# Kernel tuning notes

Measured on AMD Instinct MI355X. Metric: run time of the kernel, lower is better.

The kernel has to match this reference:

```python
import jax, jax.numpy as jnp
import numpy as np

B, S, D, H = 2, 2048, 2048, 16
HD = D // H          # 128
HALF = HD // 2       # 64
EPS = 1e-6


def setup_inputs() -> dict:
    key = jax.random.key(0)
    ks = jax.random.split(key, 10)
    x = jax.random.normal(ks[0], (B, S, D), jnp.float32)
    # RoPE frequencies: standard theta=10000, per (position, half head dim)
    inv_freq = 1.0 / (10000.0 ** (np.arange(HALF, dtype=np.float64) / HALF))
    ang = np.outer(np.arange(S, dtype=np.float64), inv_freq)  # (S, HALF)
    freqs_cos = jnp.asarray(np.cos(ang), jnp.float32)[:, None, :]  # (S,1,HALF)
    freqs_sin = jnp.asarray(np.sin(ang), jnp.float32)[:, None, :]
    sc = 0.02
    qw = jax.random.normal(ks[1], (D, D), jnp.float32) * sc
    kw = jax.random.normal(ks[2], (D, D), jnp.float32) * sc
    vw = jax.random.normal(ks[3], (D, D), jnp.float32) * sc
    ow = jax.random.normal(ks[4], (D, D), jnp.float32) * sc
    qb = jax.random.normal(ks[5], (D,), jnp.float32) * sc
    kb = jax.random.normal(ks[6], (D,), jnp.float32) * sc
    vb = jax.random.normal(ks[7], (D,), jnp.float32) * sc
    ob = jax.random.normal(ks[8], (D,), jnp.float32) * sc
    qnorm_w = jnp.ones((D,), jnp.float32)
    knorm_w = jnp.ones((D,), jnp.float32)
    return {"x": x, "freqs_cos": freqs_cos, "freqs_sin": freqs_sin,
            "qw": qw, "qb": qb, "kw": kw, "kb": kb, "vw": vw, "vb": vb,
            "ow": ow, "ob": ob, "qnorm_w": qnorm_w, "knorm_w": knorm_w}


def _rmsnorm(h, w):
    # norm in fp32 over full last dim (dim, not per-head), as in the source
    hf = h.astype(jnp.float32)
    inv = jax.lax.rsqrt(jnp.mean(hf * hf, axis=-1, keepdims=True) + EPS)
    return (hf * inv).astype(h.dtype) * w


def _rope(h, cos, sin):
    # h: (B,S,D) -> complex rotation on interleaved pairs per head
    b, s, _ = h.shape
    hp = h.reshape(b, s, H, HALF, 2)
    x1, x2 = hp[..., 0], hp[..., 1]
    c = cos[None]   # (1,S,1,HALF) broadcasts over batch & heads
    sn = sin[None]
    o1 = x1 * c - x2 * sn
    o2 = x1 * sn + x2 * c
    return jnp.stack([o1, o2], axis=-1).reshape(b, s, H * HD)


def reference(x, freqs_cos, freqs_sin, qw, qb, kw, kb, vw, vb, ow, ob, qnorm_w, knorm_w):
    q = _rope(_rmsnorm(x @ qw.T + qb, qnorm_w), freqs_cos, freqs_sin)
    k = _rope(_rmsnorm(x @ kw.T + kb, knorm_w), freqs_cos, freqs_sin)
    v = x @ vw.T + vb
    b, s, _ = x.shape
    qh = q.reshape(b, s, H, HD)
    kh = k.reshape(b, s, H, HD)
    vh = v.reshape(b, s, H, HD)
    scale = 1.0 / jnp.sqrt(jnp.float32(HD))
    att = jnp.einsum('bqhd,bkhd->bhqk', qh, kh) * scale
    p = jax.nn.softmax(att, axis=-1)
    o = jnp.einsum('bhqk,bkhd->bqhd', p, vh).reshape(b, s, D)
    return o @ ow.T + ob
```

## Files before the change

kernel.cpp:

```cpp
#include <hip/hip_runtime.h>
#include <stdint.h>

#define B_SZ 2
#define S_LEN 2048
#define D_DIM 2048
#define NHEAD 16
#define HD 128
#define HALF 64
#define MROWS (B_SZ * S_LEN)

typedef __attribute__((ext_vector_type(8))) __bf16 bf16x8;
typedef __attribute__((ext_vector_type(8))) unsigned short u16x8;
typedef __attribute__((ext_vector_type(4))) float f32x4;
typedef __attribute__((ext_vector_type(16))) float f32x16;
typedef __attribute__((ext_vector_type(4))) unsigned int u32x4;

__device__ inline unsigned short f2bf(float x) {
  union { float f; uint32_t u; } c; c.f = x;
  uint32_t r = (c.u + 0x7fffu + ((c.u >> 16) & 1u)) >> 16;
  return (unsigned short)r;
}

__device__ inline float bf2f(unsigned short b) {
  union { uint32_t u; float f; } c; c.u = (uint32_t)b << 16;
  return c.f;
}

__device__ inline void gll16(const void* g, void* l) {
  __builtin_amdgcn_global_load_lds(
      (const __attribute__((address_space(1))) void*)g,
      (__attribute__((address_space(3))) void*)l,
      16, 0, 0);
}

__global__ void cast_all(const float* __restrict__ x,
                         const float* __restrict__ qw, const float* __restrict__ kw,
                         const float* __restrict__ vw, const float* __restrict__ ow,
                         unsigned short* __restrict__ xb,
                         unsigned short* __restrict__ qwb, unsigned short* __restrict__ kwb,
                         unsigned short* __restrict__ vwb, unsigned short* __restrict__ owb) {
  const int n_x = (MROWS * D_DIM) / 4;
  const int n_w = (D_DIM * D_DIM) / 4;
  const int total = n_x + 4 * n_w;
  int i = blockIdx.x * blockDim.x + threadIdx.x;
  int stride = gridDim.x * blockDim.x;
  for (; i < total; i += stride) {
    const float* src; unsigned short* dst; int off;
    if (i < n_x) { src = x; dst = xb; off = i; }
    else {
      int j = i - n_x;
      int seg = j >> 20;
      off = j & (n_w - 1);
      src = seg == 0 ? qw : seg == 1 ? kw : seg == 2 ? vw : ow;
      dst = seg == 0 ? qwb : seg == 1 ? kwb : seg == 2 ? vwb : owb;
    }
    float4 v = reinterpret_cast<const float4*>(src)[off];
    ushort4 o;
    o.x = f2bf(v.x); o.y = f2bf(v.y); o.z = f2bf(v.z); o.w = f2bf(v.w);
    reinterpret_cast<ushort4*>(dst)[off] = o;
  }
}

template <int MODE>
__global__ __launch_bounds__(256) void gemm_bt(
    const unsigned short* __restrict__ A, const unsigned short* __restrict__ Bt,
    const float* __restrict__ bias, void* __restrict__ Cv,
    int M, int N, int K) {
  __shared__ __align__(16) unsigned short As[128 * 32];
  __shared__ __align__(16) unsigned short Bs[128 * 32];
  const int tid = threadIdx.x;
  const int lane = tid & 63;
  const int wave = tid >> 6;
  const int nbn = N >> 7;
  const int chunk = gridDim.x >> 3;
  const int lin = (blockIdx.x & 7) * chunk + (blockIdx.x >> 3);
  const int bm = lin / nbn, bn = lin - bm * nbn;
  const int wr = wave >> 1, wc = wave & 1;
  const int lm = lane & 15, lg = lane >> 4;

  f32x4 acc[4][4] = {};

  for (int k0 = 0; k0 < K; k0 += 32) {
    __syncthreads();
#pragma unroll
    for (int j = 0; j < 2; ++j) {
      int ob = wave * 2048 + j * 1024;
      int o = ob + lane * 16;
      int row = o >> 6;
      int col = (o & 63) >> 1;
      const unsigned short* ga = A + (size_t)(bm * 128 + row) * K + k0 + col;
      gll16(ga, (char*)As + ob);
      const unsigned short* gb = Bt + (size_t)(bn * 128 + row) * K + k0 + col;
      gll16(gb, (char*)Bs + ob);
    }
    __syncthreads();

    bf16x8 af[4], bfr[4];
#pragma unroll
    for (int mi = 0; mi < 4; ++mi)
      af[mi] = *reinterpret_cast<const bf16x8*>(
          &As[(wr * 64 + mi * 16 + lm) * 32 + lg * 8]);
#pragma unroll
    for (int ni = 0; ni < 4; ++ni)
      bfr[ni] = *reinterpret_cast<const bf16x8*>(
          &Bs[(wc * 64 + ni * 16 + lm) * 32 + lg * 8]);
#pragma unroll
    for (int mi = 0; mi < 4; ++mi)
#pragma unroll
      for (int ni = 0; ni < 4; ++ni)
        acc[mi][ni] = __builtin_amdgcn_mfma_f32_16x16x32_bf16(
            af[mi], bfr[ni], acc[mi][ni], 0, 0, 0);
  }

#pragma unroll
  for (int ni = 0; ni < 4; ++ni) {
    int col = bn * 128 + wc * 64 + ni * 16 + lm;
    float bv = bias[col];
    if constexpr (MODE == 2) {
      int h = col >> 7, d = col & (HD - 1);
#pragma unroll
      for (int mi = 0; mi < 4; ++mi) {
        int row0 = bm * 128 + wr * 64 + mi * 16 + lg * 4;
        int b = row0 >> 11, s0 = row0 & (S_LEN - 1);
        ushort4 o;
        o.x = f2bf(acc[mi][ni][0] + bv);
        o.y = f2bf(acc[mi][ni][1] + bv);
        o.z = f2bf(acc[mi][ni][2] + bv);
        o.w = f2bf(acc[mi][ni][3] + bv);
        unsigned short* vt = (unsigned short*)Cv;
        size_t oi = ((((size_t)(b * NHEAD + h) * (S_LEN / 64) + (s0 >> 6)) * HD + d) << 6)
                    + (s0 & 63);
        *reinterpret_cast<ushort4*>(vt + oi) = o;
      }
    } else {
#pragma unroll
      for (int mi = 0; mi < 4; ++mi) {
#pragma unroll
        for (int r = 0; r < 4; ++r) {
          int row = bm * 128 + wr * 64 + mi * 16 + lg * 4 + r;
          float v = acc[mi][ni][r] + bv;
          if constexpr (MODE == 1)
            ((unsigned short*)Cv)[(size_t)row * N + col] = f2bf(v);
          else
            ((float*)Cv)[(size_t)row * N + col] = v;
        }
      }
    }
  }
}

template <int BLOCKED>
__global__ __launch_bounds__(256) void norm_rope(
    const unsigned short* __restrict__ h, const float* __restrict__ w,
    const float* __restrict__ cosb, const float* __restrict__ sinb,
    unsigned short* __restrict__ out, float outscale) {
  const int row = blockIdx.x;
  const int pos = row & (S_LEN - 1);
  const unsigned short* hr = h + (size_t)row * D_DIM;
  const int t = threadIdx.x;
  const int d = t * 8;

  u16x8 hv = *reinterpret_cast<const u16x8*>(hr + d);
  float a[8];
#pragma unroll
  for (int i = 0; i < 8; ++i) a[i] = bf2f(hv[i]);
  float ss = 0.f;
#pragma unroll
  for (int i = 0; i < 8; ++i) ss += a[i] * a[i];
#pragma unroll
  for (int off = 32; off > 0; off >>= 1) ss += __shfl_down(ss, off);
  __shared__ float red[4];
  if ((t & 63) == 0) red[t >> 6] = ss;
  __syncthreads();
  float tot = red[0] + red[1] + red[2] + red[3];
  float inv = rsqrtf(tot * (1.0f / D_DIM) + 1e-6f) * outscale;

  const int p = (d & (HD - 1)) >> 1;
  const float* cp = cosb + pos * HALF + p;
  const float* sp = sinb + pos * HALF + p;
  const float* wp = w + d;

  float c0 = cp[0], c1 = cp[1], c2 = cp[2], c3 = cp[3];
  float s0 = sp[0], s1 = sp[1], s2 = sp[2], s3 = sp[3];
#pragma unroll
  for (int i = 0; i < 8; ++i) a[i] = a[i] * inv * wp[i];
  u16x8 o;
  o[0] = f2bf(a[0] * c0 - a[1] * s0);
  o[1] = f2bf(a[0] * s0 + a[1] * c0);
  o[2] = f2bf(a[2] * c1 - a[3] * s1);
  o[3] = f2bf(a[2] * s1 + a[3] * c1);
  o[4] = f2bf(a[4] * c2 - a[5] * s2);
  o[5] = f2bf(a[4] * s2 + a[5] * c2);
  o[6] = f2bf(a[6] * c3 - a[7] * s3);
  o[7] = f2bf(a[6] * s3 + a[7] * c3);
  if constexpr (BLOCKED) {
    int hh = t >> 4;
    int dd = d & (HD - 1);
    size_t oi = (((size_t)((row >> 11) * NHEAD + hh) * S_LEN) + pos) * HD + dd;
    *reinterpret_cast<u16x8*>(out + oi) = o;
  } else {
    *reinterpret_cast<u16x8*>(out + (size_t)row * D_DIM + d) = o;
  }
}

__global__ __launch_bounds__(512) void attn_kernel(
    const unsigned short* __restrict__ Q, const unsigned short* __restrict__ Kh,
    const unsigned short* __restrict__ Vt, unsigned short* __restrict__ O) {
  const int idx = blockIdx.x;
  const int swz = (idx & 7) * 32 + (idx >> 3);
  const int qb = swz & 7;
  const int h = (swz >> 3) & 15;
  const int b = swz >> 7;

  const int tid = threadIdx.x;
  const int lane = tid & 63;
  const int wave = tid >> 6;
  const int l31 = lane & 31;
  const int hh = lane >> 5;

  const size_t qbase = (size_t)b * S_LEN * D_DIM + (size_t)h * HD;
  const size_t hbase = (size_t)(b * NHEAD + h) * S_LEN * HD;
  const int q0w = qb * 256 + wave * 32;

  __shared__ __align__(16) unsigned short Ks[2 * 64 * 128];
  __shared__ __align__(16) unsigned short Vs[128 * 64];

  bf16x8 qf[8];
#pragma unroll
  for (int ds_ = 0; ds_ < 8; ++ds_)
    qf[ds_] = *reinterpret_cast<const bf16x8*>(
        Q + qbase + (size_t)(q0w + l31) * D_DIM + ds_ * 16 + hh * 8);

  f32x16 oacc[4] = {};
  float mrow = -1e30f, lrow = 0.f;

  const int pbase = wave * 1024 + (lane << 4);

  auto stageK = [&](int buf, int tix) {
    const unsigned short* ksrc = Kh + hbase + (size_t)tix * (64 * HD);
#pragma unroll
    for (int j = 0; j < 2; ++j) {
      int p = pbase + j * 8192;
      int kr = p >> 8;
      int kc = ((p >> 4) & 15) ^ ((kr & 7) ^ ((kr >> 3) & 7));
      gll16(ksrc + kr * 128 + kc * 8, (char*)Ks + buf * 16384 + p);
    }
  };
  auto stageV = [&](int tix) {
    const unsigned short* vsrc = Vt + hbase + (size_t)tix * (64 * HD);
#pragma unroll
    for (int j = 0; j < 2; ++j) {
      int p = pbase + j * 8192;
      int vr = p >> 7;
      int vc = ((p >> 4) & 7) ^ (((vr & 7) ^ ((vr >> 3) & 7)) & 7);
      gll16(vsrc + vr * 64 + vc * 8, (char*)Vs + p);
    }
  };

  stageK(0, 0);

  const int NT = S_LEN / 64;
  for (int t = 0; t < NT; ++t) {
    const int cur = t & 1;
    stageV(t);
    stageK(cur ^ 1, (t + 1 < NT) ? t + 1 : t);
    asm volatile("s_waitcnt vmcnt(4)" ::: "memory");
    __builtin_amdgcn_sched_barrier(0);
    __builtin_amdgcn_s_barrier();
    __builtin_amdgcn_sched_barrier(0);

    const char* kbp = (const char*)Ks + cur * 16384;
    const int fk0 = (l31 & 7) ^ ((l31 >> 3) & 7);
    const int fk1 = (l31 & 7) ^ (((l31 + 32) >> 3) & 7);
    f32x16 pA = {}, pB = {};
    __builtin_amdgcn_s_setprio(1);
#pragma unroll
    for (int ds_ = 0; ds_ < 8; ++ds_) {
      bf16x8 k0 = *reinterpret_cast<const bf16x8*>(
          kbp + l31 * 256 + (((ds_ * 2 + hh) ^ fk0) << 4));
      bf16x8 k1 = *reinterpret_cast<const bf16x8*>(
          kbp + (32 + l31) * 256 + (((ds_ * 2 + hh) ^ fk1) << 4));
      pA = __builtin_amdgcn_mfma_f32_32x32x16_bf16(k0, qf[ds_], pA, 0, 0, 0);
      pB = __builtin_amdgcn_mfma_f32_32x32x16_bf16(k1, qf[ds_], pB, 0, 0, 0);
    }
    __builtin_amdgcn_s_setprio(0);

    float m8[8];
#pragma unroll
    for (int r = 0; r < 8; ++r)
      m8[r] = fmaxf(fmaxf(pA[r], pA[r + 8]), fmaxf(pB[r], pB[r + 8]));
#pragma unroll
    for (int r = 0; r < 4; ++r) m8[r] = fmaxf(m8[r], m8[r + 4]);
    float mx = fmaxf(fmaxf(m8[0], m8[1]), fmaxf(m8[2], m8[3]));
    mx = fmaxf(mx, __shfl_xor(mx, 32));
    if (__any(mx > mrow + 8.0f)) {
      float nm = fmaxf(mrow, mx);
      float alpha = exp2f(mrow - nm);
      mrow = nm;
      lrow *= alpha;
#pragma unroll
      for (int r = 0; r < 16; ++r) {
        int qr = (r & 3) + 8 * (r >> 2) + 4 * hh;
        float av = __shfl(alpha, qr);
        oacc[0][r] *= av; oacc[1][r] *= av; oacc[2][r] *= av; oacc[3][r] *= av;
      }
    }
#pragma unroll
    for (int r = 0; r < 16; ++r) pA[r] = exp2f(pA[r] - mrow);
#pragma unroll
    for (int r = 0; r < 16; ++r) pB[r] = exp2f(pB[r] - mrow);
    float s8[8];
#pragma unroll
    for (int r = 0; r < 8; ++r)
      s8[r] = (pA[r] + pA[r + 8]) + (pB[r] + pB[r + 8]);
#pragma unroll
    for (int r = 0; r < 4; ++r) s8[r] += s8[r + 4];
    lrow += (s8[0] + s8[1]) + (s8[2] + s8[3]);

    uint32_t w[16];
#pragma unroll
    for (int gg = 0; gg < 4; ++gg) {
      uint32_t lo, hi;
      float a0 = pA[4 * gg], a1 = pA[4 * gg + 1], a2 = pA[4 * gg + 2], a3 = pA[4 * gg + 3];
      asm("v_cvt_pk_bf16_f32 %0, %1, %2" : "=v"(lo) : "v"(a0), "v"(a1));
      asm("v_cvt_pk_bf16_f32 %0, %1, %2" : "=v"(hi) : "v"(a2), "v"(a3));
      w[gg * 2] = lo; w[gg * 2 + 1] = hi;
    }
#pragma unroll
    for (int gg = 0; gg < 4; ++gg) {
      uint32_t lo, hi;
      float a0 = pB[4 * gg], a1 = pB[4 * gg + 1], a2 = pB[4 * gg + 2], a3 = pB[4 * gg + 3];
      asm("v_cvt_pk_bf16_f32 %0, %1, %2" : "=v"(lo) : "v"(a0), "v"(a1));
      asm("v_cvt_pk_bf16_f32 %0, %1, %2" : "=v"(hi) : "v"(a2), "v"(a3));
      w[8 + gg * 2] = lo; w[8 + gg * 2 + 1] = hi;
    }
    bf16x8 pa[4];
#pragma unroll
    for (int s = 0; s < 4; ++s) {
      int wb = (s >> 1) * 8 + (s & 1) * 4;
      uint32_t le = w[wb], he = w[wb + 1], lo_ = w[wb + 2], ho = w[wb + 3];
      asm("v_permlane32_swap_b32 %0, %1" : "+v"(le), "+v"(lo_));
      asm("v_permlane32_swap_b32 %0, %1" : "+v"(he), "+v"(ho));
      u32x4 fr = {le, he, lo_, ho};
      pa[s] = __builtin_bit_cast(bf16x8, fr);
    }

    asm volatile("s_waitcnt vmcnt(2)" ::: "memory");
    __builtin_amdgcn_sched_barrier(0);
    __builtin_amdgcn_s_barrier();
    __builtin_amdgcn_sched_barrier(0);

    const char* vbp = (const char*)Vs;
    __builtin_amdgcn_s_setprio(1);
#pragma unroll
    for (int db = 0; db < 4; ++db) {
      int d = db * 32 + l31;
      int fv = (d & 7) ^ ((d >> 3) & 7);
#pragma unroll
      for (int ks = 0; ks < 4; ++ks) {
        bf16x8 vv = *reinterpret_cast<const bf16x8*>(
            vbp + d * 128 + (((ks * 2 + hh) ^ fv) << 4));
        oacc[db] = __builtin_amdgcn_mfma_f32_32x32x16_bf16(pa[ks], vv, oacc[db], 0, 0, 0);
      }
    }
    __builtin_amdgcn_s_setprio(0);

    __builtin_amdgcn_sched_barrier(0);
    __builtin_amdgcn_s_barrier();
    __builtin_amdgcn_sched_barrier(0);
  }

  lrow += __shfl_xor(lrow, 32);
  float inv_[16];
#pragma unroll
  for (int r = 0; r < 16; ++r) {
    int qr = (r & 3) + 8 * (r >> 2) + 4 * hh;
    inv_[r] = 1.0f / __shfl(lrow, qr);
  }
#pragma unroll
  for (int db = 0; db < 4; ++db) {
#pragma unroll
    for (int r = 0; r < 16; ++r) {
      int qr = (r & 3) + 8 * (r >> 2) + 4 * hh;
      O[qbase + (size_t)(q0w + qr) * D_DIM + db * 32 + l31] =
          f2bf(oacc[db][r] * inv_[r]);
    }
  }
}

extern "C" void kernel_launch(void* const* d_in, const int* in_sizes, int n_in,
                              void* d_out, int out_size, void* d_ws, size_t ws_size,
                              hipStream_t stream) {
  const float* x   = (const float*)d_in[0];
  const float* fc  = (const float*)d_in[1];
  const float* fs  = (const float*)d_in[2];
  const float* qw  = (const float*)d_in[3];
  const float* qb  = (const float*)d_in[4];
  const float* kw  = (const float*)d_in[5];
  const float* kb  = (const float*)d_in[6];
  const float* vw  = (const float*)d_in[7];
  const float* vb  = (const float*)d_in[8];
  const float* ow  = (const float*)d_in[9];
  const float* ob  = (const float*)d_in[10];
  const float* qnw = (const float*)d_in[11];
  const float* knw = (const float*)d_in[12];
  float* out = (float*)d_out;

  const size_t MSD = (size_t)MROWS * D_DIM;
  const size_t WSZ = (size_t)D_DIM * D_DIM;
  char* ws = (char*)d_ws;
  unsigned short* xb   = (unsigned short*)ws; ws += MSD * 2;
  unsigned short* qwb  = (unsigned short*)ws; ws += WSZ * 2;
  unsigned short* kwb  = (unsigned short*)ws; ws += WSZ * 2;
  unsigned short* vwb  = (unsigned short*)ws; ws += WSZ * 2;
  unsigned short* owb  = (unsigned short*)ws; ws += WSZ * 2;
  unsigned short* qpre = (unsigned short*)ws; ws += MSD * 2;
  unsigned short* qb16 = (unsigned short*)ws; ws += MSD * 2;
  unsigned short* kb16 = (unsigned short*)ws; ws += MSD * 2;
  unsigned short* vt16 = (unsigned short*)ws; ws += MSD * 2;
  unsigned short* ob16 = (unsigned short*)ws; ws += MSD * 2;

  cast_all<<<2048, 256, 0, stream>>>(x, qw, kw, vw, ow, xb, qwb, kwb, vwb, owb);

  dim3 ggrid((D_DIM / 128) * (MROWS / 128));
  gemm_bt<2><<<ggrid, 256, 0, stream>>>(xb, vwb, vb, vt16, MROWS, D_DIM, D_DIM);
  gemm_bt<1><<<ggrid, 256, 0, stream>>>(xb, qwb, qb, qpre, MROWS, D_DIM, D_DIM);
  const float qscale = 0.08838834764831845f * 1.4426950408889634f;
  norm_rope<0><<<MROWS, 256, 0, stream>>>(qpre, qnw, fc, fs, qb16, qscale);
  gemm_bt<1><<<ggrid, 256, 0, stream>>>(xb, kwb, kb, qpre, MROWS, D_DIM, D_DIM);
  norm_rope<1><<<MROWS, 256, 0, stream>>>(qpre, knw, fc, fs, kb16, 1.0f);

  attn_kernel<<<dim3(S_LEN / 256 * NHEAD * B_SZ), 512, 0, stream>>>(qb16, kb16, vt16, ob16);

  gemm_bt<0><<<ggrid, 256, 0, stream>>>(ob16, owb, ob, out, MROWS, D_DIM, D_DIM);
}
```

Measured before the change: 339.6 us.

## Fuse QKV projections into one GEMM, merge norm-rope, widen attention KV tile

Runs the Q, K and V projections as a single GEMM with N=3*D by treating the contiguous qwb/kwb/vwb buffers as one weight matrix and copying the three biases into one contiguous buffer. Each output segment is routed to its own destination, with V still written in its blocked transposed layout. The two norm_rope launches become one kernel that chooses Q or K by block index. Separately, the attention kernel now processes 128 keys per iteration instead of 64, which doubles the K/V shared memory and the register use for scores in exchange for fewer barriers and loop iterations.

Result: faster. 324.3 us (-4.5%).

```diff
diff --git a/kernel.cpp b/kernel.cpp
--- a/kernel.cpp
+++ b/kernel.cpp
@@ -64,7 +64,8 @@
 template <int MODE>
 __global__ __launch_bounds__(256) void gemm_bt(
     const unsigned short* __restrict__ A, const unsigned short* __restrict__ Bt,
-    const float* __restrict__ bias, void* __restrict__ Cv,
+    const float* __restrict__ bias, void* __restrict__ C0,
+    unsigned short* __restrict__ C1, unsigned short* __restrict__ C2,
     int M, int N, int K) {
   __shared__ __align__(16) unsigned short As[128 * 32];
   __shared__ __align__(16) unsigned short Bs[128 * 32];
@@ -116,47 +117,55 @@
   for (int ni = 0; ni < 4; ++ni) {
     int col = bn * 128 + wc * 64 + ni * 16 + lm;
     float bv = bias[col];
-    if constexpr (MODE == 2) {
-      int h = col >> 7, d = col & (HD - 1);
+    if constexpr (MODE == 3) {
+      int seg = col >> 11;
+      int c2 = col & (D_DIM - 1);
 #pragma unroll
       for (int mi = 0; mi < 4; ++mi) {
         int row0 = bm * 128 + wr * 64 + mi * 16 + lg * 4;
-        int b = row0 >> 11, s0 = row0 & (S_LEN - 1);
-        ushort4 o;
-        o.x = f2bf(acc[mi][ni][0] + bv);
-        o.y = f2bf(acc[mi][ni][1] + bv);
-        o.z = f2bf(acc[mi][ni][2] + bv);
-        o.w = f2bf(acc[mi][ni][3] + bv);
-        unsigned short* vt = (unsigned short*)Cv;
-        size_t oi = ((((size_t)(b * NHEAD + h) * (S_LEN / 64) + (s0 >> 6)) * HD + d) << 6)
-                    + (s0 & 63);
-        *reinterpret_cast<ushort4*>(vt + oi) = o;
+        if (seg == 2) {
+          int b = row0 >> 11, s0 = row0 & (S_LEN - 1);
+          int h = c2 >> 7, d = c2 & (HD - 1);
+          ushort4 o;
+          o.x = f2bf(acc[mi][ni][0] + bv);
+          o.y = f2bf(acc[mi][ni][1] + bv);
+          o.z = f2bf(acc[mi][ni][2] + bv);
+          o.w = f2bf(acc[mi][ni][3] + bv);
+          size_t oi = ((((size_t)(b * NHEAD + h) * (S_LEN / 64) + (s0 >> 6)) * HD + d) << 6)
+                      + (s0 & 63);
+          *reinterpret_cast<ushort4*>(C2 + oi) = o;
+        } else {
+          unsigned short* dst = (seg == 0) ? (unsigned short*)C0 : C1;
+#pragma unroll
+          for (int r = 0; r < 4; ++r)
+            dst[(size_t)(row0 + r) * D_DIM + c2] = f2bf(acc[mi][ni][r] + bv);
+        }
       }
     } else {
+      float* out = (float*)C0;
 #pragma unroll
       for (int mi = 0; mi < 4; ++mi) {
-#pragma unroll
-        for (int r = 0; r < 4; ++r) {
-          int row = bm * 128 + wr * 64 + mi * 16 + lg * 4 + r;
-          float v = acc[mi][ni][r] + bv;
-          if constexpr (MODE == 1)
-            ((unsigned short*)Cv)[(size_t)row * N + col] = f2bf(v);
-          else
-            ((float*)Cv)[(size_t)row * N + col] = v;
-        }
-      }
-    }
-  }
-}
-
-template <int BLOCKED>
-__global__ __launch_bounds__(256) void norm_rope(
-    const unsigned short* __restrict__ h, const float* __restrict__ w,
+        int row0 = bm * 128 + wr * 64 + mi * 16 + lg * 4;
+#pragma unroll
+        for (int r = 0; r < 4; ++r)
+          out[(size_t)(row0 + r) * N + col] = acc[mi][ni][r] + bv;
+      }
+    }
+  }
+}
+
+__global__ __launch_bounds__(256) void norm_rope2(
+    const unsigned short* __restrict__ qin, const unsigned short* __restrict__ kin,
+    const float* __restrict__ qnw, const float* __restrict__ knw,
     const float* __restrict__ cosb, const float* __restrict__ sinb,
-    unsigned short* __restrict__ out, float outscale) {
-  const int row = blockIdx.x;
+    unsigned short* __restrict__ qout, unsigned short* __restrict__ kout,
+    float qscale) {
+  const int isK = blockIdx.x >> 12;
+  const int row = blockIdx.x & (MROWS - 1);
   const int pos = row & (S_LEN - 1);
-  const unsigned short* hr = h + (size_t)row * D_DIM;
+  const unsigned short* hr = (isK ? kin : qin) + (size_t)row * D_DIM;
+  const float* w = isK ? knw : qnw;
+  const float outscale = isK ? 1.0f : qscale;
   const int t = threadIdx.x;
   const int d = t * 8;
 
@@ -193,13 +202,13 @@
   o[5] = f2bf(a[4] * s2 + a[5] * c2);
   o[6] = f2bf(a[6] * c3 - a[7] * s3);
   o[7] = f2bf(a[6] * s3 + a[7] * c3);
-  if constexpr (BLOCKED) {
+  if (isK) {
     int hh = t >> 4;
     int dd = d & (HD - 1);
     size_t oi = (((size_t)((row >> 11) * NHEAD + hh) * S_LEN) + pos) * HD + dd;
-    *reinterpret_cast<u16x8*>(out + oi) = o;
+    *reinterpret_cast<u16x8*>(kout + oi) = o;
   } else {
-    *reinterpret_cast<u16x8*>(out + (size_t)row * D_DIM + d) = o;
+    *reinterpret_cast<u16x8*>(qout + (size_t)row * D_DIM + d) = o;
   }
 }
 
@@ -222,8 +231,8 @@
   const size_t hbase = (size_t)(b * NHEAD + h) * S_LEN * HD;
   const int q0w = qb * 256 + wave * 32;
 
-  __shared__ __align__(16) unsigned short Ks[2 * 64 * 128];
-  __shared__ __align__(16) unsigned short Vs[128 * 64];
+  __shared__ __align__(16) unsigned short Ks[2 * 128 * 128];
+  __shared__ __align__(16) unsigned short Vs[2 * 128 * 64];
 
   bf16x8 qf[8];
 #pragma unroll
@@ -237,61 +246,62 @@
   const int pbase = wave * 1024 + (lane << 4);
 
   auto stageK = [&](int buf, int tix) {
-    const unsigned short* ksrc = Kh + hbase + (size_t)tix * (64 * HD);
-#pragma unroll
-    for (int j = 0; j < 2; ++j) {
+    const unsigned short* ksrc = Kh + hbase + (size_t)tix * (128 * HD);
+#pragma unroll
+    for (int j = 0; j < 4; ++j) {
       int p = pbase + j * 8192;
       int kr = p >> 8;
       int kc = ((p >> 4) & 15) ^ ((kr & 7) ^ ((kr >> 3) & 7));
-      gll16(ksrc + kr * 128 + kc * 8, (char*)Ks + buf * 16384 + p);
+      gll16(ksrc + kr * 128 + kc * 8, (char*)Ks + buf * 32768 + p);
     }
   };
   auto stageV = [&](int tix) {
-    const unsigned short* vsrc = Vt + hbase + (size_t)tix * (64 * HD);
-#pragma unroll
-    for (int j = 0; j < 2; ++j) {
+    const unsigned short* vsrc = Vt + hbase + (size_t)tix * (128 * HD);
+#pragma unroll
+    for (int j = 0; j < 4; ++j) {
       int p = pbase + j * 8192;
-      int vr = p >> 7;
+      int vr = (p & 16383) >> 7;
       int vc = ((p >> 4) & 7) ^ (((vr & 7) ^ ((vr >> 3) & 7)) & 7);
-      gll16(vsrc + vr * 64 + vc * 8, (char*)Vs + p);
+      gll16(vsrc + (p >> 14) * (64 * HD) + vr * 64 + vc * 8, (char*)Vs + p);
     }
   };
 
   stageK(0, 0);
 
-  const int NT = S_LEN / 64;
+  const int NT = S_LEN / 128;
   for (int t = 0; t < NT; ++t) {
     const int cur = t & 1;
     stageV(t);
     stageK(cur ^ 1, (t + 1 < NT) ? t + 1 : t);
-    asm volatile("s_waitcnt vmcnt(4)" ::: "memory");
+    asm volatile("s_waitcnt vmcnt(8)" ::: "memory");
     __builtin_amdgcn_sched_barrier(0);
     __builtin_amdgcn_s_barrier();
     __builtin_amdgcn_sched_barrier(0);
 
-    const char* kbp = (const char*)Ks + cur * 16384;
-    const int fk0 = (l31 & 7) ^ ((l31 >> 3) & 7);
-    const int fk1 = (l31 & 7) ^ (((l31 + 32) >> 3) & 7);
-    f32x16 pA = {}, pB = {};
+    const char* kbp = (const char*)Ks + cur * 32768;
+    f32x16 sc[4] = {};
     __builtin_amdgcn_s_setprio(1);
 #pragma unroll
     for (int ds_ = 0; ds_ < 8; ++ds_) {
-      bf16x8 k0 = *reinterpret_cast<const bf16x8*>(
-          kbp + l31 * 256 + (((ds_ * 2 + hh) ^ fk0) << 4));
-      bf16x8 k1 = *reinterpret_cast<const bf16x8*>(
-          kbp + (32 + l31) * 256 + (((ds_ * 2 + hh) ^ fk1) << 4));
-      pA = __builtin_amdgcn_mfma_f32_32x32x16_bf16(k0, qf[ds_], pA, 0, 0, 0);
-      pB = __builtin_amdgcn_mfma_f32_32x32x16_bf16(k1, qf[ds_], pB, 0, 0, 0);
+#pragma unroll
+      for (int j = 0; j < 4; ++j) {
+        int r = j * 32 + l31;
+        bf16x8 kf = *reinterpret_cast<const bf16x8*>(
+            kbp + r * 256 + (((ds_ * 2 + hh) ^ ((r & 7) ^ ((r >> 3) & 7))) << 4));
+        sc[j] = __builtin_amdgcn_mfma_f32_32x32x16_bf16(kf, qf[ds_], sc[j], 0, 0, 0);
+      }
     }
     __builtin_amdgcn_s_setprio(0);
 
-    float m8[8];
-#pragma unroll
-    for (int r = 0; r < 8; ++r)
-      m8[r] = fmaxf(fmaxf(pA[r], pA[r + 8]), fmaxf(pB[r], pB[r + 8]));
-#pragma unroll
-    for (int r = 0; r < 4; ++r) m8[r] = fmaxf(m8[r], m8[r + 4]);
-    float mx = fmaxf(fmaxf(m8[0], m8[1]), fmaxf(m8[2], m8[3]));
+    float m0[16];
+#pragma unroll
+    for (int r = 0; r < 16; ++r)
+      m0[r] = fmaxf(fmaxf(sc[0][r], sc[1][r]), fmaxf(sc[2][r], sc[3][r]));
+#pragma unroll
+    for (int r = 0; r < 8; ++r) m0[r] = fmaxf(m0[r], m0[r + 8]);
+#pragma unroll
+    for (int r = 0; r < 4; ++r) m0[r] = fmaxf(m0[r], m0[r + 4]);
+    float mx = fmaxf(fmaxf(m0[0], m0[1]), fmaxf(m0[2], m0[3]));
     mx = fmaxf(mx, __shfl_xor(mx, 32));
     if (__any(mx > mrow + 8.0f)) {
       float nm = fmaxf(mrow, mx);
@@ -306,37 +316,35 @@
       }
     }
 #pragma unroll
-    for (int r = 0; r < 16; ++r) pA[r] = exp2f(pA[r] - mrow);
-#pragma unroll
-    for (int r = 0; r < 16; ++r) pB[r] = exp2f(pB[r] - mrow);
-    float s8[8];
-#pragma unroll
-    for (int r = 0; r < 8; ++r)
-      s8[r] = (pA[r] + pA[r + 8]) + (pB[r] + pB[r + 8]);
-#pragma unroll
-    for (int r = 0; r < 4; ++r) s8[r] += s8[r + 4];
-    lrow += (s8[0] + s8[1]) + (s8[2] + s8[3]);
-
-    uint32_t w[16];
-#pragma unroll
-    for (int gg = 0; gg < 4; ++gg) {
-      uint32_t lo, hi;
-      float a0 = pA[4 * gg], a1 = pA[4 * gg + 1], a2 = pA[4 * gg + 2], a3 = pA[4 * gg + 3];
-      asm("v_cvt_pk_bf16_f32 %0, %1, %2" : "=v"(lo) : "v"(a0), "v"(a1));
-      asm("v_cvt_pk_bf16_f32 %0, %1, %2" : "=v"(hi) : "v"(a2), "v"(a3));
-      w[gg * 2] = lo; w[gg * 2 + 1] = hi;
-    }
-#pragma unroll
-    for (int gg = 0; gg < 4; ++gg) {
-      uint32_t lo, hi;
-      float a0 = pB[4 * gg], a1 = pB[4 * gg + 1], a2 = pB[4 * gg + 2], a3 = pB[4 * gg + 3];
-      asm("v_cvt_pk_bf16_f32 %0, %1, %2" : "=v"(lo) : "v"(a0), "v"(a1));
-      asm("v_cvt_pk_bf16_f32 %0, %1, %2" : "=v"(hi) : "v"(a2), "v"(a3));
-      w[8 + gg * 2] = lo; w[8 + gg * 2 + 1] = hi;
-    }
-    bf16x8 pa[4];
-#pragma unroll
-    for (int s = 0; s < 4; ++s) {
+    for (int j = 0; j < 4; ++j)
+#pragma unroll
+      for (int r = 0; r < 16; ++r) sc[j][r] = exp2f(sc[j][r] - mrow);
+    float s0[16];
+#pragma unroll
+    for (int r = 0; r < 16; ++r)
+      s0[r] = (sc[0][r] + sc[1][r]) + (sc[2][r] + sc[3][r]);
+#pragma unroll
+    for (int r = 0; r < 8; ++r) s0[r] += s0[r + 8];
+#pragma unroll
+    for (int r = 0; r < 4; ++r) s0[r] += s0[r + 4];
+    lrow += (s0[0] + s0[1]) + (s0[2] + s0[3]);
+
+    uint32_t w[32];
+#pragma unroll
+    for (int X = 0; X < 4; ++X) {
+#pragma unroll
+      for (int g = 0; g < 4; ++g) {
+        uint32_t lo, hi;
+        float a0 = sc[X][4 * g], a1 = sc[X][4 * g + 1];
+        float a2 = sc[X][4 * g + 2], a3 = sc[X][4 * g + 3];
+        asm("v_cvt_pk_bf16_f32 %0, %1, %2" : "=v"(lo) : "v"(a0), "v"(a1));
+        asm("v_cvt_pk_bf16_f32 %0, %1, %2" : "=v"(hi) : "v"(a2), "v"(a3));
+        w[X * 8 + g * 2] = lo; w[X * 8 + g * 2 + 1] = hi;
+      }
+    }
+    bf16x8 pa[8];
+#pragma unroll
+    for (int s = 0; s < 8; ++s) {
       int wb = (s >> 1) * 8 + (s & 1) * 4;
       uint32_t le = w[wb], he = w[wb + 1], lo_ = w[wb + 2], ho = w[wb + 3];
       asm("v_permlane32_swap_b32 %0, %1" : "+v"(le), "+v"(lo_));
@@ -345,7 +353,7 @@
       pa[s] = __builtin_bit_cast(bf16x8, fr);
     }
 
-    asm volatile("s_waitcnt vmcnt(2)" ::: "memory");
+    asm volatile("s_waitcnt vmcnt(4)" ::: "memory");
     __builtin_amdgcn_sched_barrier(0);
     __builtin_amdgcn_s_barrier();
     __builtin_amdgcn_sched_barrier(0);
@@ -355,11 +363,11 @@
 #pragma unroll
     for (int db = 0; db < 4; ++db) {
       int d = db * 32 + l31;
-      int fv = (d & 7) ^ ((d >> 3) & 7);
-#pragma unroll
-      for (int ks = 0; ks < 4; ++ks) {
+      int fv = ((d & 7) ^ ((d >> 3) & 7)) & 7;
+#pragma unroll
+      for (int ks = 0; ks < 8; ++ks) {
         bf16x8 vv = *reinterpret_cast<const bf16x8*>(
-            vbp + d * 128 + (((ks * 2 + hh) ^ fv) << 4));
+            vbp + (ks >> 2) * 16384 + d * 128 + ((((ks & 3) * 2 + hh) ^ fv) << 4));
         oacc[db] = __builtin_amdgcn_mfma_f32_32x32x16_bf16(pa[ks], vv, oacc[db], 0, 0, 0);
       }
     }
@@ -414,23 +422,28 @@
   unsigned short* kwb  = (unsigned short*)ws; ws += WSZ * 2;
   unsigned short* vwb  = (unsigned short*)ws; ws += WSZ * 2;
   unsigned short* owb  = (unsigned short*)ws; ws += WSZ * 2;
+  float*          cbias = (float*)ws;         ws += 3 * D_DIM * 4;
   unsigned short* qpre = (unsigned short*)ws; ws += MSD * 2;
+  unsigned short* kpre = (unsigned short*)ws; ws += MSD * 2;
   unsigned short* qb16 = (unsigned short*)ws; ws += MSD * 2;
   unsigned short* kb16 = (unsigned short*)ws; ws += MSD * 2;
   unsigned short* vt16 = (unsigned short*)ws; ws += MSD * 2;
   unsigned short* ob16 = (unsigned short*)ws; ws += MSD * 2;
 
   cast_all<<<2048, 256, 0, stream>>>(x, qw, kw, vw, ow, xb, qwb, kwb, vwb, owb);
-
-  dim3 ggrid((D_DIM / 128) * (MROWS / 128));
-  gemm_bt<2><<<ggrid, 256, 0, stream>>>(xb, vwb, vb, vt16, MROWS, D_DIM, D_DIM);
-  gemm_bt<1><<<ggrid, 256, 0, stream>>>(xb, qwb, qb, qpre, MROWS, D_DIM, D_DIM);
+  hipMemcpyAsync(cbias,              qb, D_DIM * sizeof(float), hipMemcpyDeviceToDevice, stream);
+  hipMemcpyAsync(cbias + D_DIM,      kb, D_DIM * sizeof(float), hipMemcpyDeviceToDevice, stream);
+  hipMemcpyAsync(cbias + 2 * D_DIM,  vb, D_DIM * sizeof(float), hipMemcpyDeviceToDevice, stream);
+
+  gemm_bt<3><<<dim3((MROWS / 128) * (3 * D_DIM / 128)), 256, 0, stream>>>(
+      xb, qwb, cbias, qpre, kpre, vt16, MROWS, 3 * D_DIM, D_DIM);
+
   const float qscale = 0.08838834764831845f * 1.4426950408889634f;
-  norm_rope<0><<<MROWS, 256, 0, stream>>>(qpre, qnw, fc, fs, qb16, qscale);
-  gemm_bt<1><<<ggrid, 256, 0, stream>>>(xb, kwb, kb, qpre, MROWS, D_DIM, D_DIM);
-  norm_rope<1><<<MROWS, 256, 0, stream>>>(qpre, knw, fc, fs, kb16, 1.0f);
+  norm_rope2<<<2 * MROWS, 256, 0, stream>>>(qpre, kpre, qnw, knw, fc, fs,
+                                            qb16, kb16, qscale);
 
   attn_kernel<<<dim3(S_LEN / 256 * NHEAD * B_SZ), 512, 0, stream>>>(qb16, kb16, vt16, ob16);
 
-  gemm_bt<0><<<ggrid, 256, 0, stream>>>(ob16, owb, ob, out, MROWS, D_DIM, D_DIM);
-}
+  gemm_bt<0><<<dim3((MROWS / 128) * (D_DIM / 128)), 256, 0, stream>>>(
+      ob16, owb, ob, out, nullptr, nullptr, MROWS, D_DIM, D_DIM);
+}
```
